# Kernel tuning notes

Measured on AMD Instinct MI355X. Metric: run time of the kernel, lower is better.

## Reference

```python
import jax, jax.numpy as jnp
import numpy as np

B, S, IN, D, HID, H, K, YD = 4, 2048, 64, 128, 400, 4, 20, 4
WHICH_OUT = 0
ALPHAS = jnp.array([0.05, 0.06, 0.08, 0.1, 0.12, 0.14, 0.15, 0.17, 0.19, 0.2,
                    0.21, 0.23, 0.25, 0.3, 0.35, 0.38, 0.4, 0.45], dtype=jnp.float32)  # 18 alphas


def _mlp(x, W1, b1, W2, b2, W3, b3, W4, b4):
    # FcModel encoder: in -> 400 -> 400 -> 400 -> out, ReLU hidden, linear head
    h = jax.nn.relu(x @ W1 + b1)
    h = jax.nn.relu(h @ W2 + b2)
    h = jax.nn.relu(h @ W3 + b3)
    return h @ W4 + b4


def _ln(x, g, b):
    mu = jnp.mean(x, axis=-1, keepdims=True)
    var = jnp.var(x, axis=-1, keepdims=True)
    return (x - mu) * jax.lax.rsqrt(var + 1e-5) * g + b


def setup_inputs() -> dict:
    key = jax.random.key(0)
    ks = jax.random.split(key, 16)
    w = lambda k, shape: 0.05 * jax.random.normal(k, shape, dtype=jnp.float32)
    return {
        'X_ctx_true': jax.random.normal(ks[0], (B, S, IN), dtype=jnp.float32),
        'X_ctx_sim':  jax.random.normal(ks[1], (B, S, IN), dtype=jnp.float32),
        'errors':     jax.random.normal(ks[2], (B, S, YD), dtype=jnp.float32),
        'y':          jax.random.normal(ks[3], (B, S, YD), dtype=jnp.float32),
        'y_pred':     jax.random.normal(ks[4], (B, S, YD), dtype=jnp.float32),
        'W1': w(ks[5], (IN, HID)),  'b1': jnp.zeros((HID,), jnp.float32),
        'W2': w(ks[6], (HID, HID)), 'b2': jnp.zeros((HID,), jnp.float32),
        'W3': w(ks[7], (HID, HID)), 'b3': jnp.zeros((HID,), jnp.float32),
        'W4': w(ks[8], (HID, D)),   'b4': jnp.zeros((D,), jnp.float32),
        'Wq': w(ks[9], (D, H * D)), 'bq': jnp.zeros((H * D,), jnp.float32),
        'Wk': w(ks[10], (D, H * D)), 'bk': jnp.zeros((H * D,), jnp.float32),
        'g_q': jnp.ones((D,), jnp.float32), 'beta_q': jnp.zeros((D,), jnp.float32),
        'g_k': jnp.ones((D,), jnp.float32), 'beta_k': jnp.zeros((D,), jnp.float32),
    }


def reference(X_ctx_true, X_ctx_sim, errors, y, y_pred,
              W1, b1, W2, b2, W3, b3, W4, b4,
              Wq, bq, Wk, bk, g_q, beta_q, g_k, beta_k):
    err_w = errors[..., WHICH_OUT]                      # [B,S]
    enc_true = _mlp(X_ctx_true, W1, b1, W2, b2, W3, b3, W4, b4)  # [B,S,D]
    enc_sim = _mlp(X_ctx_sim, W1, b1, W2, b2, W3, b3, W4, b4)    # [B,S,D]

    # Hopfield association: LayerNorm on state (query) and stored (key) patterns,
    # per-head projection to hidden_size=D, scaled dot product, diag mask, softmax.
    q = (_ln(enc_true, g_q, beta_q) @ Wq + bq).reshape(B, S, H, D)
    k = (_ln(enc_sim, g_k, beta_k) @ Wk + bk).reshape(B, S, H, D)
    scores = jnp.einsum('bshd,bmhd->bhsm', q, k) / jnp.sqrt(jnp.float32(D))
    diag = jnp.eye(S, dtype=bool)
    scores = jnp.where(diag[None, None], -jnp.inf, scores)
    assoc = jax.nn.softmax(scores, axis=-1)             # [B,H,S,M]

    # topk sampling of memory slots, gather corresponding errors
    _, idx = jax.lax.top_k(assoc, K)                    # [B,H,S,K]
    sel = err_w[jnp.arange(B)[:, None, None, None], idx]  # [B,H,S,K]

    # quantiles over samples for all alphas at once (torch.quantile = linear interp)
    betas = ALPHAS / 2.0
    q_low = jnp.quantile(sel, betas, axis=-1)           # [A,B,H,S]
    q_high = jnp.quantile(sel, 1.0 - ALPHAS + betas, axis=-1)  # [A,B,H,S]

    yp = y_pred[..., WHICH_OUT]                         # [B,S]
    y_low = q_low + yp[None, :, None, :]                # [A,B,H,S]
    y_high = q_high + yp[None, :, None, :]

    # mean-quantile MSE score, per head then averaged
    mean_err = jnp.concatenate([q_low, q_high], axis=0).mean(axis=0)  # [B,H,S]
    pred_adj = mean_err + yp[:, None, :]                # [B,H,S]
    y_true = y[..., WHICH_OUT]                          # [B,S]
    scores_per_head = jnp.mean((y_true[:, None, :] - pred_adj) ** 2, axis=(0, 2))  # [H]
    score = jnp.mean(scores_per_head)

    to_out = lambda a: jnp.transpose(a, (2, 1, 0, 3))[..., None]  # [A,B,H,S]->[H,B,A,S,1]
    return (score, y, y_pred, to_out(y_low), to_out(y_high),
            errors[..., WHICH_OUT:WHICH_OUT + 1], to_out(q_low), to_out(q_high))
```

## Files before the change

### kernel.cpp

```cpp
#include <hip/hip_runtime.h>
#include <hip/hip_bf16.h>
#include <math.h>


#define SS 2048
#define ROWS 16
#define AST 400

typedef short short8v __attribute__((ext_vector_type(8)));
typedef float float4v __attribute__((ext_vector_type(4)));
typedef float float2v __attribute__((ext_vector_type(2)));

__constant__ float c_alphas[18] = {0.05f,0.06f,0.08f,0.1f,0.12f,0.14f,0.15f,0.17f,
                                   0.19f,0.2f,0.21f,0.23f,0.25f,0.3f,0.35f,0.38f,0.4f,0.45f};

#define OFF_Y      1
#define OFF_YPRED  32769
#define OFF_YLOW   65537ll
#define OFF_YHIGH  655361ll
#define OFF_ERR    1245185ll
#define OFF_QLOW   1253377ll
#define OFF_QHIGH  1843201ll

__device__ inline short f2bf_s(float f) {
    __hip_bfloat16 h = __float2bfloat16(f);
    return __builtin_bit_cast(short, h);
}
__device__ inline unsigned mono(float f) {
    unsigned u = __builtin_bit_cast(unsigned, f);
    return (u & 0x80000000u) ? ~u : (u | 0x80000000u);
}
__device__ inline unsigned umin_(unsigned a, unsigned b) { return a < b ? a : b; }
__device__ inline unsigned umax_(unsigned a, unsigned b) { return a > b ? a : b; }


template<int IN_W, int NCC>
__device__ __forceinline__ void mlp_layer_acc(
    const float* __restrict__ W, const float* __restrict__ act,
    const int w, const int t, float (&acc)[ROWS][2])
{
    int jm[2];
    #pragma unroll
    for (int cc = 0; cc < NCC; ++cc) {
        const int j = w*128 + cc*64 + t;
        jm[cc] = (j < 400) ? j : 399;
    }
    #pragma unroll
    for (int r = 0; r < ROWS; ++r)
        #pragma unroll
        for (int cc = 0; cc < NCC; ++cc) acc[r][cc] = 0.f;

    #pragma unroll 2
    for (int i4 = 0; i4 < IN_W/4; ++i4) {
        float wv[4][2];
        #pragma unroll
        for (int jj = 0; jj < 4; ++jj)
            #pragma unroll
            for (int cc = 0; cc < NCC; ++cc)
                wv[jj][cc] = W[(i4*4 + jj)*400 + jm[cc]];
        #pragma unroll
        for (int r = 0; r < ROWS; ++r) {
            const float4v xv = *(const float4v*)(act + r*AST + i4*4);
            #pragma unroll
            for (int jj = 0; jj < 4; ++jj)
                #pragma unroll
                for (int cc = 0; cc < NCC; ++cc)
                    acc[r][cc] = fmaf(xv[jj], wv[jj][cc], acc[r][cc]);
        }
    }
}

__device__ __forceinline__ void mlp_layer_store(
    const float* __restrict__ b, float* __restrict__ act,
    const int w, const int t, const int ncc, const float (&acc)[ROWS][2])
{
    #pragma unroll
    for (int cc = 0; cc < 2; ++cc) {
        const int j = w*128 + cc*64 + t;
        if (cc < ncc && j < 400) {
            const float bv = b[j];
            #pragma unroll
            for (int r = 0; r < ROWS; ++r)
                act[r*AST + j] = fmaxf(acc[r][cc] + bv, 0.f);
        }
    }
}

__global__ __launch_bounds__(256, 4) void k_mlp(
    const float* __restrict__ Xt, const float* __restrict__ Xs,
    const float* __restrict__ W1, const float* __restrict__ b1,
    const float* __restrict__ W2, const float* __restrict__ b2,
    const float* __restrict__ W3, const float* __restrict__ b3,
    const float* __restrict__ W4, const float* __restrict__ b4,
    const float* __restrict__ Wq, const float* __restrict__ bq,
    const float* __restrict__ Wk, const float* __restrict__ bk,
    const float* __restrict__ g_q, const float* __restrict__ beta_q,
    const float* __restrict__ g_k, const float* __restrict__ beta_k,
    float* __restrict__ qf, float* __restrict__ kf,
    __hip_bfloat16* __restrict__ khi)
{
    __shared__ float act[ROWS*AST];

    const int tid  = threadIdx.x;
    const int t    = tid & 63;
    const int w    = tid >> 6;
    const int bi   = blockIdx.x;
    const int half = bi >> 9;
    const int rbase = (bi & 511) * ROWS;
    const float* X = half ? Xs : Xt;

    #pragma unroll
    for (int u = 0; u < (ROWS*64)/256; ++u) {
        const int e = u*256 + tid;
        act[(e >> 6)*AST + (e & 63)] = X[(size_t)rbase*64 + e];
    }
    __syncthreads();

    float acc[ROWS][2];
    const int ncc = (w == 3) ? 1 : 2;

    if (w == 3) mlp_layer_acc<64,1>(W1, act, w, t, acc);
    else        mlp_layer_acc<64,2>(W1, act, w, t, acc);
    __syncthreads();
    mlp_layer_store(b1, act, w, t, ncc, acc);
    __syncthreads();

    if (w == 3) mlp_layer_acc<400,1>(W2, act, w, t, acc);
    else        mlp_layer_acc<400,2>(W2, act, w, t, acc);
    __syncthreads();
    mlp_layer_store(b2, act, w, t, ncc, acc);
    __syncthreads();

    if (w == 3) mlp_layer_acc<400,1>(W3, act, w, t, acc);
    else        mlp_layer_acc<400,2>(W3, act, w, t, acc);
    __syncthreads();
    mlp_layer_store(b3, act, w, t, ncc, acc);
    __syncthreads();

    float2v a4[4];
    #pragma unroll
    for (int rr = 0; rr < 4; ++rr) a4[rr] = (float2v){0.f, 0.f};
    #pragma unroll 2
    for (int i4 = 0; i4 < 100; ++i4) {
        float wv0[4], wv1[4];
        #pragma unroll
        for (int jj = 0; jj < 4; ++jj) {
            wv0[jj] = W4[(i4*4 + jj)*128 + t];
            wv1[jj] = W4[(i4*4 + jj)*128 + 64 + t];
        }
        #pragma unroll
        for (int rr = 0; rr < 4; ++rr) {
            const float4v xv = *(const float4v*)(act + (w*4 + rr)*AST + i4*4);
            #pragma unroll
            for (int jj = 0; jj < 4; ++jj) {
                a4[rr][0] = fmaf(xv[jj], wv0[jj], a4[rr][0]);
                a4[rr][1] = fmaf(xv[jj], wv1[jj], a4[rr][1]);
            }
        }
    }
    {
        const float b40 = b4[t], b41 = b4[64 + t];
        #pragma unroll
        for (int rr = 0; rr < 4; ++rr) { a4[rr][0] += b40; a4[rr][1] += b41; }
    }
    __syncthreads();

    {
        const float* g  = half ? g_k : g_q;
        const float* be = half ? beta_k : beta_q;
        const float gl0 = g[t],  gl1 = g[64 + t];
        const float bl0 = be[t], bl1 = be[64 + t];
        #pragma unroll
        for (int rr = 0; rr < 4; ++rr) {
            float s = a4[rr][0] + a4[rr][1];
            #pragma unroll
            for (int o = 32; o > 0; o >>= 1) s += __shfl_xor(s, o);
            const float mu = s * (1.f/128.f);
            const float d0 = a4[rr][0] - mu, d1 = a4[rr][1] - mu;
            float vs = d0*d0 + d1*d1;
            #pragma unroll
            for (int o = 32; o > 0; o >>= 1) vs += __shfl_xor(vs, o);
            const float rstd = rsqrtf(vs * (1.f/128.f) + 1e-5f);
            act[(w*4 + rr)*128 + t]      = d0*rstd*gl0 + bl0;
            act[(w*4 + rr)*128 + 64 + t] = d1*rstd*gl1 + bl1;
        }
    }
    __syncthreads();

    {
        const float* Wp = half ? Wk : Wq;
        const float* bp = half ? bk : bq;
        float* of = half ? kf : qf;

        float accp[ROWS][2];
        #pragma unroll
        for (int r = 0; r < ROWS; ++r) { accp[r][0] = 0.f; accp[r][1] = 0.f; }
        #pragma unroll 2
        for (int i4 = 0; i4 < 32; ++i4) {
            float wv[4][2];
            #pragma unroll
            for (int jj = 0; jj < 4; ++jj)
                #pragma unroll
                for (int cc = 0; cc < 2; ++cc)
                    wv[jj][cc] = Wp[(i4*4 + jj)*512 + w*128 + cc*64 + t];
            #pragma unroll
            for (int r = 0; r < ROWS; ++r) {
                const float4v xv = *(const float4v*)(act + r*128 + i4*4);
                #pragma unroll
                for (int jj = 0; jj < 4; ++jj)
                    #pragma unroll
                    for (int cc = 0; cc < 2; ++cc)
                        accp[r][cc] = fmaf(xv[jj], wv[jj][cc], accp[r][cc]);
            }
        }

        float bpv[2];
        bpv[0] = bp[w*128 + t];
        bpv[1] = bp[w*128 + 64 + t];
        #pragma unroll
        for (int r = 0; r < ROWS; ++r) {
            const int gidx = rbase + r;
            const int bb = gidx >> 11, s = gidx & 2047;
            const int T = s >> 4, m16s = s & 15;
            #pragma unroll
            for (int cc = 0; cc < 2; ++cc) {
                const int j  = w*128 + cc*64 + t;
                const int hh = j >> 7, d = j & 127;
                const float v = accp[r][cc] + bpv[cc];
                const size_t dst = ((size_t)(bb*4 + hh)*2048 + s)*128 + d;
                of[dst] = v;
                if (half) {
                    const int ks = d >> 5, qd = (d & 31) >> 3, jj = d & 7;
                    const size_t so = (size_t)(bb*4 + hh)*262144
                                    + (size_t)T*2048 + ks*512 + qd*128 + m16s*8 + jj;
                    khi[so] = __float2bfloat16(v);
                }
            }
        }
    }
}

__global__ __launch_bounds__(256, 4) void k_scan(
    const float* __restrict__ qf, const __hip_bfloat16* __restrict__ khi,
    unsigned* __restrict__ wsk)
{
    __shared__ unsigned kd[64*97];

    const int tid   = threadIdx.x;
    const int stile = blockIdx.x;
    const int hb    = blockIdx.y;
    const int mq    = blockIdx.z;

    const int lane = tid & 63;
    const int w    = tid >> 6;
    const int m16  = lane & 15;
    const int quad = lane >> 4;

    const size_t slab = (size_t)hb * 2048;
    const __hip_bfloat16* slabp = khi + (size_t)hb * 262144;

    const int sg_my = stile*64 + w*16 + m16;

    short8v bq_[4];
    {
        const float* qp = qf + (slab + sg_my)*128 + quad*8;
        #pragma unroll
        for (int ks = 0; ks < 4; ++ks) {
            const float4 x0 = *(const float4*)(qp + ks*32);
            const float4 x1 = *(const float4*)(qp + ks*32 + 4);
            short8v tt;
            tt[0]=f2bf_s(x0.x); tt[1]=f2bf_s(x0.y); tt[2]=f2bf_s(x0.z); tt[3]=f2bf_s(x0.w);
            tt[4]=f2bf_s(x1.x); tt[5]=f2bf_s(x1.y); tt[6]=f2bf_s(x1.z); tt[7]=f2bf_s(x1.w);
            bq_[ks] = tt;
        }
    }

    unsigned KA[12], KB[12];
    #pragma unroll
    for (int n = 0; n < 12; ++n) { KA[n] = 0u; KB[n] = 0u; }

    #pragma unroll 1
    for (int cti = 0; cti < 32; ++cti) {
        const int T = mq*32 + cti;
        const __hip_bfloat16* kp = slabp + (size_t)T*2048 + lane*8;
        float4v acc = (float4v){0.f,0.f,0.f,0.f};
        #pragma unroll
        for (int ks = 0; ks < 4; ++ks) {
            const short8v ka = *(const short8v*)(kp + ks*512);
            acc = __builtin_amdgcn_mfma_f32_16x16x32_bf16(ka, bq_[ks], acc, 0, 0, 0);
        }
        const int cb = T*16 + quad*4;
        #pragma unroll
        for (int ph = 0; ph < 2; ++ph) {
            {
                const int m = cb + ph;
                unsigned key = (mono(acc[ph]) & 0xFFFFF800u) | (unsigned)m;
                key = (m == sg_my) ? 0u : key;
                KA[0] = umax_(KA[0], key);
                #pragma unroll
                for (int i = 0; i < 11; ++i) {
                    const unsigned a = KA[i], c = KA[i+1];
                    KA[i]   = umin_(a, c);
                    KA[i+1] = umax_(a, c);
                }
            }
            {
                const int m = cb + 2 + ph;
                unsigned key = (mono(acc[2+ph]) & 0xFFFFF800u) | (unsigned)m;
                key = (m == sg_my) ? 0u : key;
                KB[0] = umax_(KB[0], key);
                #pragma unroll
                for (int i = 0; i < 11; ++i) {
                    const unsigned a = KB[i], c = KB[i+1];
                    KB[i]   = umin_(a, c);
                    KB[i+1] = umax_(a, c);
                }
            }
        }
    }

    const int rr = w*16 + m16;
    #pragma unroll
    for (int n = 0; n < 12; ++n) {
        kd[rr*97 + (quad*2 + 0)*12 + n] = KA[11 - n];
        kd[rr*97 + (quad*2 + 1)*12 + n] = KB[11 - n];
    }
    __syncthreads();

    if (quad == 0) {
        const unsigned* R = &kd[rr*97];
        int q0=0,q1=0,q2=0,q3=0,q4=0,q5=0,q6=0,q7=0;
        const size_t base = (size_t)hb*2048 + stile*64 + rr;
        #pragma unroll 1
        for (int n = 0; n < 24; ++n) {
            const unsigned h0 = (q0<12)?R[  0+q0]:0u;
            const unsigned h1 = (q1<12)?R[ 12+q1]:0u;
            const unsigned h2 = (q2<12)?R[ 24+q2]:0u;
            const unsigned h3 = (q3<12)?R[ 36+q3]:0u;
            const unsigned h4 = (q4<12)?R[ 48+q4]:0u;
            const unsigned h5 = (q5<12)?R[ 60+q5]:0u;
            const unsigned h6 = (q6<12)?R[ 72+q6]:0u;
            const unsigned h7 = (q7<12)?R[ 84+q7]:0u;
            unsigned bv = h0; int bs = 0;
            if (h1 > bv) { bv = h1; bs = 1; }
            if (h2 > bv) { bv = h2; bs = 2; }
            if (h3 > bv) { bv = h3; bs = 3; }
            if (h4 > bv) { bv = h4; bs = 4; }
            if (h5 > bv) { bv = h5; bs = 5; }
            if (h6 > bv) { bv = h6; bs = 6; }
            if (h7 > bv) { bv = h7; bs = 7; }
            q0 += (bs==0); q1 += (bs==1); q2 += (bs==2); q3 += (bs==3);
            q4 += (bs==4); q5 += (bs==5); q6 += (bs==6); q7 += (bs==7);
            wsk[(size_t)(mq*24 + n)*32768 + base] = bv;
        }
    }
}

__global__ __launch_bounds__(256, 4) void k_select(
    const float* __restrict__ qf, const float* __restrict__ kf,
    const unsigned* __restrict__ wsk,
    const float* __restrict__ errors, const float* __restrict__ y,
    const float* __restrict__ y_pred,
    float* __restrict__ out, float* __restrict__ hacc)
{
    __shared__ unsigned kd[64*4*25];
    __shared__ unsigned short cb[64*33];
    __shared__ float es[64*33];
    __shared__ float ebuf[64*21];

    const int tid   = threadIdx.x;
    const int stile = blockIdx.x;
    const int hb    = blockIdx.y;
    const int b     = hb >> 2;
    const int h     = hb & 3;

    const int lane = tid & 63;
    const int w    = tid >> 6;
    const int m16  = lane & 15;
    const int quad = lane >> 4;
    const int rr   = w*16 + m16;
    const int sg   = stile*64 + rr;

    const size_t base = (size_t)hb*2048 + sg;
    #pragma unroll 1
    for (int n = 0; n < 24; ++n)
        kd[(rr*4 + quad)*25 + n] = wsk[(size_t)(quad*24 + n)*32768 + base];
    __syncthreads();

    if (quad == 0) {
        const unsigned* L0 = &kd[(rr*4 + 0)*25];
        const unsigned* L1 = &kd[(rr*4 + 1)*25];
        const unsigned* L2 = &kd[(rr*4 + 2)*25];
        const unsigned* L3 = &kd[(rr*4 + 3)*25];
        int p0 = 0, p1 = 0, p2 = 0, p3 = 0;
        #pragma unroll 1
        for (int n = 0; n < 32; ++n) {
            const unsigned h0 = (p0 < 24) ? L0[p0] : 0u;
            const unsigned h1 = (p1 < 24) ? L1[p1] : 0u;
            const unsigned h2 = (p2 < 24) ? L2[p2] : 0u;
            const unsigned h3 = (p3 < 24) ? L3[p3] : 0u;
            unsigned bv = h0; int bs = 0;
            if (h1 > bv) { bv = h1; bs = 1; }
            if (h2 > bv) { bv = h2; bs = 2; }
            if (h3 > bv) { bv = h3; bs = 3; }
            if (bs == 0) ++p0; else if (bs == 1) ++p1; else if (bs == 2) ++p2; else ++p3;
            cb[rr*33 + n] = (unsigned short)(bv & 0x7FFu);
        }
    }
    __syncthreads();

    const size_t slab = (size_t)hb * 2048;
    const float* qrow_p = qf + (slab + sg)*128;
    float4 qseg[8];
    #pragma unroll
    for (int u = 0; u < 8; ++u)
        qseg[u] = *(const float4*)(qrow_p + quad*4 + u*16);
    const float* kslab = kf + slab*128;
    #pragma unroll 1
    for (int n = 0; n < 32; ++n) {
        const int col = cb[rr*33 + n];
        const float* kc = kslab + (size_t)col*128 + quad*4;
        float2v s01 = (float2v){0.f, 0.f}, s23 = (float2v){0.f, 0.f};
        #pragma unroll
        for (int u = 0; u < 8; ++u) {
            const float4 kv = *(const float4*)(kc + u*16);
            s01 = __builtin_elementwise_fma((float2v){qseg[u].x, qseg[u].y},
                                            (float2v){kv.x, kv.y}, s01);
            s23 = __builtin_elementwise_fma((float2v){qseg[u].z, qseg[u].w},
                                            (float2v){kv.z, kv.w}, s23);
        }
        float v = (s01[0] + s01[1]) + (s23[0] + s23[1]);
        v += __shfl_xor(v, 16);
        v += __shfl_xor(v, 32);
        if (quad == 0) es[rr*33 + n] = v;
    }

    float sq = 0.f;
    if (quad == 0) {
        float* e = &ebuf[rr*21];
        #pragma unroll 1
        for (int k = 0; k < 20; ++k) {
            float best = -INFINITY; int bc = 4096, bj = 0;
            #pragma unroll 1
            for (int j = 0; j < 32; ++j) {
                const float v = es[rr*33 + j];
                const int c = cb[rr*33 + j];
                if (v > best || (v == best && c < bc)) { best = v; bc = c; bj = j; }
            }
            es[rr*33 + bj] = -INFINITY;
            e[k] = errors[((size_t)(b*SS + bc))*4];
        }
        #pragma unroll 1
        for (int a = 1; a < 20; ++a) {
            const float v = e[a];
            int n = a;
            while (n > 0 && e[n-1] > v) { e[n] = e[n-1]; --n; }
            e[n] = v;
        }
        const float yp = y_pred[((size_t)(b*SS + sg))*4];
        const float yt = y[((size_t)(b*SS + sg))*4];
        float msum = 0.f;
        const size_t obase = ((size_t)(h*4 + b)*18)*2048 + sg;
        #pragma unroll 1
        for (int a = 0; a < 18; ++a) {
            const float alpha = c_alphas[a];
            const float beta  = 0.5f*alpha;
            const float pl = beta * 19.f;
            const int   il = (int)pl;
            const float fl = pl - (float)il;
            const float ql = e[il]*(1.f-fl) + e[il+1]*fl;
            const float qq = (1.f - alpha) + beta;
            const float ph = qq * 19.f;
            const int   ih = (int)ph;
            const float fh = ph - (float)ih;
            const float qh = e[ih]*(1.f-fh) + e[ih+1]*fh;
            msum += ql + qh;
            const size_t oidx = obase + (size_t)a*2048;
            out[OFF_YLOW  + oidx] = ql + yp;
            out[OFF_YHIGH + oidx] = qh + yp;
            out[OFF_QLOW  + oidx] = ql;
            out[OFF_QHIGH + oidx] = qh;
        }
        const float me = msum * (1.f/36.f);
        const float dd = yt - (me + yp);
        sq = dd*dd;
    }
    #pragma unroll
    for (int o = 32; o > 0; o >>= 1) sq += __shfl_xor(sq, o);
    if (lane == 0) atomicAdd(&hacc[h], sq);
}

__global__ void k_init(float* __restrict__ hacc) {
    if (threadIdx.x < 4) hacc[threadIdx.x] = 0.f;
}

__global__ __launch_bounds__(256) void k_finalize(
    const float* __restrict__ y, const float* __restrict__ y_pred,
    const float* __restrict__ errors, const float* __restrict__ hacc,
    float* __restrict__ out)
{
    const int i = blockIdx.x*256 + threadIdx.x;
    if (i == 0)
        out[0] = (hacc[0]+hacc[1]+hacc[2]+hacc[3]) * (1.f/32768.f);
    if (i < 32768)      out[OFF_Y + i] = y[i];
    else if (i < 65536) out[OFF_YPRED + (i - 32768)] = y_pred[i - 32768];
    else if (i < 73728) { const int j = i - 65536; out[OFF_ERR + j] = errors[(size_t)j*4]; }
}

extern "C" void kernel_launch(void* const* d_in, const int* in_sizes, int n_in,
                              void* d_out, int out_size, void* d_ws, size_t ws_size,
                              hipStream_t stream)
{
    const float* Xt     = (const float*)d_in[0];
    const float* Xs     = (const float*)d_in[1];
    const float* errors = (const float*)d_in[2];
    const float* y      = (const float*)d_in[3];
    const float* y_pred = (const float*)d_in[4];
    const float* W1 = (const float*)d_in[5];   const float* b1 = (const float*)d_in[6];
    const float* W2 = (const float*)d_in[7];   const float* b2 = (const float*)d_in[8];
    const float* W3 = (const float*)d_in[9];   const float* b3 = (const float*)d_in[10];
    const float* W4 = (const float*)d_in[11];  const float* b4 = (const float*)d_in[12];
    const float* Wq = (const float*)d_in[13];  const float* bq = (const float*)d_in[14];
    const float* Wk = (const float*)d_in[15];  const float* bk = (const float*)d_in[16];
    const float* g_q    = (const float*)d_in[17];
    const float* beta_q = (const float*)d_in[18];
    const float* g_k    = (const float*)d_in[19];
    const float* beta_k = (const float*)d_in[20];

    float* out  = (float*)d_out;
    char*  base = (char*)d_ws;
    const size_t SLAB = (size_t)16*2048*128;
    float* hacc = (float*)base;
    float* qf   = (float*)(base + 256);
    float* kf   = qf + SLAB;
    __hip_bfloat16* khi = (__hip_bfloat16*)(kf + SLAB);
    unsigned* wsk = (unsigned*)(khi + SLAB);

    k_init<<<1, 64, 0, stream>>>(hacc);
    k_mlp<<<1024, 256, 0, stream>>>(Xt, Xs, W1,b1,W2,b2,W3,b3,W4,b4,
                                    Wq,bq,Wk,bk,g_q,beta_q,g_k,beta_k,
                                    qf, kf, khi);
    k_scan<<<dim3(32,16,4), 256, 0, stream>>>(qf, khi, wsk);
    k_select<<<dim3(32,16), 256, 0, stream>>>(qf, kf, wsk, errors, y, y_pred, out, hacc);
    k_finalize<<<288, 256, 0, stream>>>(y, y_pred, errors, hacc, out);
}
```

Baseline: 610.7 us.

## Halve MLP rows per block, vectorize weight columns, rotate tail-slice across waves

The MLP kernel now handles 8 rows per block instead of 16, with twice as many blocks and launch bounds raised to 8 blocks per CU for more occupancy. Each lane now owns two adjacent output columns, loaded and stored as float2. The short 16-column tail slice is rotated across waves by block index so the idle wave is not always the same one. Projection outputs and the bf16 key copy are written as packed pairs. In exchange, weights are re-read from cache twice as often per row, and each weight load is reused across fewer rows.

```diff
diff --git a/kernel.cpp b/kernel.cpp
--- a/kernel.cpp
+++ b/kernel.cpp
@@ -4,7 +4,7 @@
 
 
 #define SS 2048
-#define ROWS 16
+#define ROWS 8
 #define AST 400
 
 typedef short short8v __attribute__((ext_vector_type(8)));
@@ -34,59 +34,81 @@
 __device__ inline unsigned umax_(unsigned a, unsigned b) { return a > b ? a : b; }
 
 
-template<int IN_W, int NCC>
-__device__ __forceinline__ void mlp_layer_acc(
+template<int IN_W, int WST, int AS>
+__device__ __forceinline__ void layer_acc2(
     const float* __restrict__ W, const float* __restrict__ act,
-    const int w, const int t, float (&acc)[ROWS][2])
-{
-    int jm[2];
-    #pragma unroll
-    for (int cc = 0; cc < NCC; ++cc) {
-        const int j = w*128 + cc*64 + t;
-        jm[cc] = (j < 400) ? j : 399;
-    }
-    #pragma unroll
-    for (int r = 0; r < ROWS; ++r)
-        #pragma unroll
-        for (int cc = 0; cc < NCC; ++cc) acc[r][cc] = 0.f;
-
+    const int c0, float (&acc)[ROWS][2])
+{
+    #pragma unroll
+    for (int r = 0; r < ROWS; ++r) { acc[r][0] = 0.f; acc[r][1] = 0.f; }
     #pragma unroll 2
     for (int i4 = 0; i4 < IN_W/4; ++i4) {
-        float wv[4][2];
+        float2 wv[4];
         #pragma unroll
         for (int jj = 0; jj < 4; ++jj)
+            wv[jj] = *(const float2*)(W + (i4*4 + jj)*WST + c0);
+        #pragma unroll
+        for (int r = 0; r < ROWS; ++r) {
+            const float4v xv = *(const float4v*)(act + r*AS + i4*4);
             #pragma unroll
-            for (int cc = 0; cc < NCC; ++cc)
-                wv[jj][cc] = W[(i4*4 + jj)*400 + jm[cc]];
+            for (int jj = 0; jj < 4; ++jj) {
+                acc[r][0] = fmaf(xv[jj], wv[jj].x, acc[r][0]);
+                acc[r][1] = fmaf(xv[jj], wv[jj].y, acc[r][1]);
+            }
+        }
+    }
+}
+
+template<int IN_W, int WST, int AS>
+__device__ __forceinline__ void layer_acc1(
+    const float* __restrict__ W, const float* __restrict__ act,
+    const int jm, float (&acc)[ROWS][2])
+{
+    #pragma unroll
+    for (int r = 0; r < ROWS; ++r) acc[r][0] = 0.f;
+    #pragma unroll 2
+    for (int i4 = 0; i4 < IN_W/4; ++i4) {
+        float wv[4];
+        #pragma unroll
+        for (int jj = 0; jj < 4; ++jj)
+            wv[jj] = W[(i4*4 + jj)*WST + jm];
         #pragma unroll
         for (int r = 0; r < ROWS; ++r) {
-            const float4v xv = *(const float4v*)(act + r*AST + i4*4);
+            const float4v xv = *(const float4v*)(act + r*AS + i4*4);
             #pragma unroll
             for (int jj = 0; jj < 4; ++jj)
-                #pragma unroll
-                for (int cc = 0; cc < NCC; ++cc)
-                    acc[r][cc] = fmaf(xv[jj], wv[jj][cc], acc[r][cc]);
-        }
-    }
-}
-
-__device__ __forceinline__ void mlp_layer_store(
+                acc[r][0] = fmaf(xv[jj], wv[jj], acc[r][0]);
+        }
+    }
+}
+
+__device__ __forceinline__ void store2(
     const float* __restrict__ b, float* __restrict__ act,
-    const int w, const int t, const int ncc, const float (&acc)[ROWS][2])
-{
-    #pragma unroll
-    for (int cc = 0; cc < 2; ++cc) {
-        const int j = w*128 + cc*64 + t;
-        if (cc < ncc && j < 400) {
-            const float bv = b[j];
-            #pragma unroll
-            for (int r = 0; r < ROWS; ++r)
-                act[r*AST + j] = fmaxf(acc[r][cc] + bv, 0.f);
-        }
-    }
-}
-
-__global__ __launch_bounds__(256, 4) void k_mlp(
+    const int c0, const float (&acc)[ROWS][2])
+{
+    const float2 bb = *(const float2*)(b + c0);
+    #pragma unroll
+    for (int r = 0; r < ROWS; ++r) {
+        float2 v;
+        v.x = fmaxf(acc[r][0] + bb.x, 0.f);
+        v.y = fmaxf(acc[r][1] + bb.y, 0.f);
+        *(float2*)(&act[r*AST + c0]) = v;
+    }
+}
+
+__device__ __forceinline__ void store1(
+    const float* __restrict__ b, float* __restrict__ act,
+    const int jm, const bool real, const float (&acc)[ROWS][2])
+{
+    if (real) {
+        const float bv = b[jm];
+        #pragma unroll
+        for (int r = 0; r < ROWS; ++r)
+            act[r*AST + jm] = fmaxf(acc[r][0] + bv, 0.f);
+    }
+}
+
+__global__ __launch_bounds__(256, 8) void k_mlp(
     const float* __restrict__ Xt, const float* __restrict__ Xs,
     const float* __restrict__ W1, const float* __restrict__ b1,
     const float* __restrict__ W2, const float* __restrict__ b2,
@@ -105,9 +127,14 @@
     const int t    = tid & 63;
     const int w    = tid >> 6;
     const int bi   = blockIdx.x;
-    const int half = bi >> 9;
-    const int rbase = (bi & 511) * ROWS;
+    const int half = bi >> 10;
+    const int rbase = (bi & 1023) * ROWS;
     const float* X = half ? Xs : Xt;
+
+    const int sl  = (w + bi) & 3;
+    const int c0  = sl*128 + 2*t;
+    const int jm  = (t < 16) ? (384 + t) : 399;
+    const bool s3 = (sl == 3);
 
     #pragma unroll
     for (int u = 0; u < (ROWS*64)/256; ++u) {
@@ -117,29 +144,31 @@
     __syncthreads();
 
     float acc[ROWS][2];
-    const int ncc = (w == 3) ? 1 : 2;
-
-    if (w == 3) mlp_layer_acc<64,1>(W1, act, w, t, acc);
-    else        mlp_layer_acc<64,2>(W1, act, w, t, acc);
-    __syncthreads();
-    mlp_layer_store(b1, act, w, t, ncc, acc);
-    __syncthreads();
-
-    if (w == 3) mlp_layer_acc<400,1>(W2, act, w, t, acc);
-    else        mlp_layer_acc<400,2>(W2, act, w, t, acc);
-    __syncthreads();
-    mlp_layer_store(b2, act, w, t, ncc, acc);
-    __syncthreads();
-
-    if (w == 3) mlp_layer_acc<400,1>(W3, act, w, t, acc);
-    else        mlp_layer_acc<400,2>(W3, act, w, t, acc);
-    __syncthreads();
-    mlp_layer_store(b3, act, w, t, ncc, acc);
-    __syncthreads();
-
-    float2v a4[4];
-    #pragma unroll
-    for (int rr = 0; rr < 4; ++rr) a4[rr] = (float2v){0.f, 0.f};
+
+    if (s3) layer_acc1<64,400,AST>(W1, act, jm, acc);
+    else    layer_acc2<64,400,AST>(W1, act, c0, acc);
+    __syncthreads();
+    if (s3) store1(b1, act, jm, t < 16, acc);
+    else    store2(b1, act, c0, acc);
+    __syncthreads();
+
+    if (s3) layer_acc1<400,400,AST>(W2, act, jm, acc);
+    else    layer_acc2<400,400,AST>(W2, act, c0, acc);
+    __syncthreads();
+    if (s3) store1(b2, act, jm, t < 16, acc);
+    else    store2(b2, act, c0, acc);
+    __syncthreads();
+
+    if (s3) layer_acc1<400,400,AST>(W3, act, jm, acc);
+    else    layer_acc2<400,400,AST>(W3, act, c0, acc);
+    __syncthreads();
+    if (s3) store1(b3, act, jm, t < 16, acc);
+    else    store2(b3, act, c0, acc);
+    __syncthreads();
+
+    float2v a4[2];
+    #pragma unroll
+    for (int rr = 0; rr < 2; ++rr) a4[rr] = (float2v){0.f, 0.f};
     #pragma unroll 2
     for (int i4 = 0; i4 < 100; ++i4) {
         float wv0[4], wv1[4];
@@ -149,8 +178,8 @@
             wv1[jj] = W4[(i4*4 + jj)*128 + 64 + t];
         }
         #pragma unroll
-        for (int rr = 0; rr < 4; ++rr) {
-            const float4v xv = *(const float4v*)(act + (w*4 + rr)*AST + i4*4);
+        for (int rr = 0; rr < 2; ++rr) {
+            const float4v xv = *(const float4v*)(act + (w*2 + rr)*AST + i4*4);
             #pragma unroll
             for (int jj = 0; jj < 4; ++jj) {
                 a4[rr][0] = fmaf(xv[jj], wv0[jj], a4[rr][0]);
@@ -161,7 +190,7 @@
     {
         const float b40 = b4[t], b41 = b4[64 + t];
         #pragma unroll
-        for (int rr = 0; rr < 4; ++rr) { a4[rr][0] += b40; a4[rr][1] += b41; }
+        for (int rr = 0; rr < 2; ++rr) { a4[rr][0] += b40; a4[rr][1] += b41; }
     }
     __syncthreads();
 
@@ -171,7 +200,7 @@
         const float gl0 = g[t],  gl1 = g[64 + t];
         const float bl0 = be[t], bl1 = be[64 + t];
         #pragma unroll
-        for (int rr = 0; rr < 4; ++rr) {
+        for (int rr = 0; rr < 2; ++rr) {
             float s = a4[rr][0] + a4[rr][1];
             #pragma unroll
             for (int o = 32; o > 0; o >>= 1) s += __shfl_xor(s, o);
@@ -181,8 +210,8 @@
             #pragma unroll
             for (int o = 32; o > 0; o >>= 1) vs += __shfl_xor(vs, o);
             const float rstd = rsqrtf(vs * (1.f/128.f) + 1e-5f);
-            act[(w*4 + rr)*128 + t]      = d0*rstd*gl0 + bl0;
-            act[(w*4 + rr)*128 + 64 + t] = d1*rstd*gl1 + bl1;
+            act[(w*2 + rr)*128 + t]      = d0*rstd*gl0 + bl0;
+            act[(w*2 + rr)*128 + 64 + t] = d1*rstd*gl1 + bl1;
         }
     }
     __syncthreads();
@@ -193,48 +222,27 @@
         float* of = half ? kf : qf;
 
         float accp[ROWS][2];
-        #pragma unroll
-        for (int r = 0; r < ROWS; ++r) { accp[r][0] = 0.f; accp[r][1] = 0.f; }
-        #pragma unroll 2
-        for (int i4 = 0; i4 < 32; ++i4) {
-            float wv[4][2];
-            #pragma unroll
-            for (int jj = 0; jj < 4; ++jj)
-                #pragma unroll
-                for (int cc = 0; cc < 2; ++cc)
-                    wv[jj][cc] = Wp[(i4*4 + jj)*512 + w*128 + cc*64 + t];
-            #pragma unroll
-            for (int r = 0; r < ROWS; ++r) {
-                const float4v xv = *(const float4v*)(act + r*128 + i4*4);
-                #pragma unroll
-                for (int jj = 0; jj < 4; ++jj)
-                    #pragma unroll
-                    for (int cc = 0; cc < 2; ++cc)
-                        accp[r][cc] = fmaf(xv[jj], wv[jj][cc], accp[r][cc]);
-            }
-        }
-
-        float bpv[2];
-        bpv[0] = bp[w*128 + t];
-        bpv[1] = bp[w*128 + 64 + t];
+        layer_acc2<128,512,128>(Wp, act, c0, accp);
+
+        const float2 bpp = *(const float2*)(bp + c0);
+        const int hh = c0 >> 7;
+        const int d0 = c0 & 127;
+        const int ks = d0 >> 5, qd = (d0 & 31) >> 3, jj0 = d0 & 7;
         #pragma unroll
         for (int r = 0; r < ROWS; ++r) {
             const int gidx = rbase + r;
-            const int bb = gidx >> 11, s = gidx & 2047;
+            const int bB = gidx >> 11, s = gidx & 2047;
             const int T = s >> 4, m16s = s & 15;
-            #pragma unroll
-            for (int cc = 0; cc < 2; ++cc) {
-                const int j  = w*128 + cc*64 + t;
-                const int hh = j >> 7, d = j & 127;
-                const float v = accp[r][cc] + bpv[cc];
-                const size_t dst = ((size_t)(bb*4 + hh)*2048 + s)*128 + d;
-                of[dst] = v;
-                if (half) {
-                    const int ks = d >> 5, qd = (d & 31) >> 3, jj = d & 7;
-                    const size_t so = (size_t)(bb*4 + hh)*262144
-                                    + (size_t)T*2048 + ks*512 + qd*128 + m16s*8 + jj;
-                    khi[so] = __float2bfloat16(v);
-                }
+            const float v0 = accp[r][0] + bpp.x;
+            const float v1 = accp[r][1] + bpp.y;
+            const size_t dst = ((size_t)(bB*4 + hh)*2048 + s)*128 + d0;
+            *(float2*)(of + dst) = make_float2(v0, v1);
+            if (half) {
+                const size_t so = (size_t)(bB*4 + hh)*262144
+                                + (size_t)T*2048 + ks*512 + qd*128 + m16s*8 + jj0;
+                const unsigned pk = (unsigned)(unsigned short)f2bf_s(v0)
+                                  | ((unsigned)(unsigned short)f2bf_s(v1) << 16);
+                *reinterpret_cast<unsigned*>(khi + so) = pk;
             }
         }
     }
@@ -537,7 +545,7 @@
     unsigned* wsk = (unsigned*)(khi + SLAB);
 
     k_init<<<1, 64, 0, stream>>>(hacc);
-    k_mlp<<<1024, 256, 0, stream>>>(Xt, Xs, W1,b1,W2,b2,W3,b3,W4,b4,
+    k_mlp<<<2048, 256, 0, stream>>>(Xt, Xs, W1,b1,W2,b2,W3,b3,W4,b4,
                                     Wq,bq,Wk,bk,g_q,beta_q,g_k,beta_k,
                                     qf, kf, khi);
     k_scan<<<dim3(32,16,4), 256, 0, stream>>>(qf, khi, wsk);
```

Measured after the change: 678.0 us. +11.0%, slower.
